# Kernel tuning notes

Measured on AMD Instinct MI355X. Metric: run time of the kernel, lower is better.

Reference implementation:

```python
import jax, jax.numpy as jnp
import numpy as np

T, B, N = 2048, 32, 1024   # time, batch, dan_hidden_size
H = 8                      # multihead_size
N2 = 128                   # attention_hidden_size
K = N // H                 # N_H = 128 per-head dim
K2 = N2 // H               # N2_H = 16 per-head attention dim


def setup_inputs() -> dict:
    key = jax.random.key(0)
    ks = jax.random.split(key, 10)
    s_n = 1.0 / np.sqrt(N)
    s_k = 1.0 / np.sqrt(K)
    s_k2 = 1.0 / np.sqrt(K2)
    return {
        "hyp": jax.random.normal(ks[0], (T, B, N), dtype=jnp.float32),
        # H independent per-head linears N -> K, stacked: (H, K, N)
        "Wmh": jax.random.uniform(ks[1], (H, K, N), minval=-s_n, maxval=s_n, dtype=jnp.float32),
        "bmh": jax.random.uniform(ks[2], (H, K), minval=-s_n, maxval=s_n, dtype=jnp.float32),
        # shared W: K -> K2
        "W": jax.random.uniform(ks[3], (K2, K), minval=-s_k, maxval=s_k, dtype=jnp.float32),
        "bW": jax.random.uniform(ks[4], (K2,), minval=-s_k, maxval=s_k, dtype=jnp.float32),
        # shared W_m: K -> K2
        "Wm": jax.random.uniform(ks[5], (K2, K), minval=-s_k, maxval=s_k, dtype=jnp.float32),
        "bWm": jax.random.uniform(ks[6], (K2,), minval=-s_k, maxval=s_k, dtype=jnp.float32),
        # shared W_h: K2 -> 1
        "Wh": jax.random.uniform(ks[7], (K2,), minval=-s_k2, maxval=s_k2, dtype=jnp.float32),
        "bWh": jax.random.uniform(ks[8], (), minval=-s_k2, maxval=s_k2, dtype=jnp.float32),
        "dan_hidden_size": N,
        "attention_hidden_size": N2,
        "multihead_size": H,
    }


def reference(hyp, Wmh, bmh, W, bW, Wm, bWm, Wh, bWh,
              dan_hidden_size, attention_hidden_size, multihead_size):
    # Per-head projections, all heads at once: (B, T, H, K)
    X = jnp.einsum('tbn,hkn->bthk', hyp, Wmh) + bmh
    # mean over time (original x.mean(0)): (B, H, K)
    m = X.mean(axis=1)
    # tanh-gated additive scoring: (B, T, H, K2)
    g = jnp.tanh(jnp.einsum('bthk,qk->bthq', X, W) + bW) \
        * jnp.tanh(jnp.einsum('bhk,qk->bhq', m, Wm) + bWm)[:, None]
    # scalar score per (b, t, h), softmax over time
    s = jnp.einsum('bthq,q->bth', g, Wh) + bWh
    a = jax.nn.softmax(s, axis=1)                       # (B, T, H)
    # attention-weighted sum over time: (B, H, K)
    c = jnp.einsum('bth,bthk->bhk', a, X)
    # concat heads along feature dim (head-major order, matches torch.cat)
    Bsz = c.shape[0]
    return c.reshape(Bsz, -1)                            # (B, N)
```

## Files before the change

### kernel.cpp

```cpp
#include <hip/hip_runtime.h>
#include <hip/hip_bf16.h>

#define T_DIM 2048
#define B_DIM 32
#define N_DIM 1024
#define H_DIM 8
#define K_DIM 128
#define Q_DIM 16

typedef __bf16 bf16x8 __attribute__((ext_vector_type(8)));
typedef __bf16 bf16x4 __attribute__((ext_vector_type(4)));
typedef float  f32x4  __attribute__((ext_vector_type(4)));

__device__ inline bf16x8 cvt8(float4 a, float4 b) {
    bf16x8 r;
    r[0] = (__bf16)a.x; r[1] = (__bf16)a.y; r[2] = (__bf16)a.z; r[3] = (__bf16)a.w;
    r[4] = (__bf16)b.x; r[5] = (__bf16)b.y; r[6] = (__bf16)b.z; r[7] = (__bf16)b.w;
    return r;
}

__global__ __launch_bounds__(256)
void cvt_f32_bf16(const float* __restrict__ s, __bf16* __restrict__ d)
{
    const long i = ((long)blockIdx.x * 256 + threadIdx.x) * 8;
    float4 a = *(const float4*)(s + i);
    float4 b = *(const float4*)(s + i + 4);
    *(bf16x8*)(d + i) = cvt8(a, b);
}

__global__ __launch_bounds__(512, 2)
void gemm_x_8ph(const __bf16* __restrict__ A, const __bf16* __restrict__ Bw,
                const float* __restrict__ bias, __bf16* __restrict__ X)
{
    __shared__ __bf16 lds[2][2][16384];

    const int tid  = threadIdx.x;
    const int lane = tid & 63;
    const int w    = tid >> 6;
    const int wm   = w >> 2;
    const int wn   = w & 3;

    const int bid  = blockIdx.x;
    const int wgid = (bid & 7) * 128 + (bid >> 3);
    const int bm   = wgid >> 2;
    const int bn   = wgid & 3;
    const long row0 = (long)bm * 256;
    const long col0 = (long)bn * 256;

    const int srow = w * 8 + (lane >> 3);
    const int scol = ((lane & 7) ^ (lane >> 3)) * 8;
    const __bf16* Ag = A  + (row0 + srow) * 1024 + scol;
    const __bf16* Bg = Bw + (col0 + srow) * 1024 + scol;
    const int ldst = w * 512;

    auto stage = [&](int kt, int sl) {
        const long ko = (long)kt * 64;
        #pragma unroll
        for (int j = 0; j < 4; ++j)
            __builtin_amdgcn_global_load_lds(
                (const __attribute__((address_space(1))) void*)(Ag + (long)j * 65536 + ko),
                (__attribute__((address_space(3))) void*)(&lds[sl][0][j * 4096 + ldst]),
                16, 0, 0);
        #pragma unroll
        for (int j = 0; j < 4; ++j)
            __builtin_amdgcn_global_load_lds(
                (const __attribute__((address_space(1))) void*)(Bg + (long)j * 65536 + ko),
                (__attribute__((address_space(3))) void*)(&lds[sl][1][j * 4096 + ldst]),
                16, 0, 0);
    };

    const int fr = lane & 15;
    const int g2 = lane >> 4;
    const int x7 = lane & 7;

    f32x4 acc[8][4];
    #pragma unroll
    for (int i = 0; i < 8; ++i)
        #pragma unroll
        for (int j = 0; j < 4; ++j)
            acc[i][j] = f32x4{0.f, 0.f, 0.f, 0.f};

    stage(0, 0);
    stage(1, 1);
    asm volatile("s_waitcnt vmcnt(8)" ::: "memory");
    __builtin_amdgcn_s_barrier();

    #pragma unroll 1
    for (int i = 0; i < 16; ++i) {
        const int s = i & 1;
        const __bf16* Al = &lds[s][0][0];
        const __bf16* Bl = &lds[s][1][0];

        bf16x8 a0[4][2], a1[4][2], b0[4], b1[4];

        #pragma unroll
        for (int mi = 0; mi < 4; ++mi) {
            const int row = wm * 128 + mi * 16 + fr;
            a0[mi][0] = *(const bf16x8*)(Al + row * 64 + ((g2    ) ^ x7) * 8);
            a0[mi][1] = *(const bf16x8*)(Al + row * 64 + ((4 + g2) ^ x7) * 8);
        }
        #pragma unroll
        for (int ni = 0; ni < 4; ++ni) {
            const int row = wn * 64 + ni * 16 + fr;
            b0[ni] = *(const bf16x8*)(Bl + row * 64 + ((g2) ^ x7) * 8);
        }
        __builtin_amdgcn_s_barrier();
        __builtin_amdgcn_s_setprio(1);
        #pragma unroll
        for (int mi = 0; mi < 4; ++mi)
            #pragma unroll
            for (int ni = 0; ni < 4; ++ni)
                acc[mi][ni] = __builtin_amdgcn_mfma_f32_16x16x32_bf16(a0[mi][0], b0[ni], acc[mi][ni], 0, 0, 0);
        __builtin_amdgcn_s_setprio(0);
        __builtin_amdgcn_s_barrier();

        #pragma unroll
        for (int ni = 0; ni < 4; ++ni) {
            const int row = wn * 64 + ni * 16 + fr;
            b1[ni] = *(const bf16x8*)(Bl + row * 64 + ((4 + g2) ^ x7) * 8);
        }
        __builtin_amdgcn_s_barrier();
        __builtin_amdgcn_s_setprio(1);
        #pragma unroll
        for (int mi = 0; mi < 4; ++mi)
            #pragma unroll
            for (int ni = 0; ni < 4; ++ni)
                acc[mi][ni] = __builtin_amdgcn_mfma_f32_16x16x32_bf16(a0[mi][1], b1[ni], acc[mi][ni], 0, 0, 0);
        __builtin_amdgcn_s_setprio(0);
        __builtin_amdgcn_s_barrier();

        #pragma unroll
        for (int mi = 0; mi < 4; ++mi) {
            const int row = wm * 128 + (mi + 4) * 16 + fr;
            a1[mi][0] = *(const bf16x8*)(Al + row * 64 + ((g2    ) ^ x7) * 8);
            a1[mi][1] = *(const bf16x8*)(Al + row * 64 + ((4 + g2) ^ x7) * 8);
        }
        __builtin_amdgcn_s_barrier();
        __builtin_amdgcn_s_setprio(1);
        #pragma unroll
        for (int mi = 0; mi < 4; ++mi)
            #pragma unroll
            for (int ni = 0; ni < 4; ++ni)
                acc[mi + 4][ni] = __builtin_amdgcn_mfma_f32_16x16x32_bf16(a1[mi][0], b0[ni], acc[mi + 4][ni], 0, 0, 0);
        __builtin_amdgcn_s_setprio(0);
        __builtin_amdgcn_s_barrier();

        if (i < 14) stage(i + 2, s);
        __builtin_amdgcn_s_barrier();
        __builtin_amdgcn_s_setprio(1);
        #pragma unroll
        for (int mi = 0; mi < 4; ++mi)
            #pragma unroll
            for (int ni = 0; ni < 4; ++ni)
                acc[mi + 4][ni] = __builtin_amdgcn_mfma_f32_16x16x32_bf16(a1[mi][1], b1[ni], acc[mi + 4][ni], 0, 0, 0);
        __builtin_amdgcn_s_setprio(0);
        if (i < 14) { asm volatile("s_waitcnt vmcnt(8)" ::: "memory"); }
        else        { asm volatile("s_waitcnt vmcnt(0)" ::: "memory"); }
        __builtin_amdgcn_s_barrier();
    }

    const int g4 = lane >> 4;
    #pragma unroll
    for (int ni = 0; ni < 4; ++ni) {
        const long col = col0 + wn * 64 + ni * 16 + fr;
        const float bv = bias[col];
        #pragma unroll
        for (int mi = 0; mi < 8; ++mi) {
            #pragma unroll
            for (int r = 0; r < 4; ++r) {
                const long row = row0 + wm * 128 + mi * 16 + g4 * 4 + r;
                X[row * 1024 + col] = (__bf16)(acc[mi][ni][r] + bv);
            }
        }
    }
}

__global__ __launch_bounds__(256, 2)
void gemm_x_kernel(const float* __restrict__ A, const float* __restrict__ Bw,
                   const float* __restrict__ bias, __bf16* __restrict__ X)
{
    __shared__ __bf16 As[128 * 32];
    __shared__ __bf16 Bs[128 * 32];
    const int tid  = threadIdx.x;
    const int lane = tid & 63;
    const int w    = tid >> 6;
    const int wr   = w >> 1;
    const int wc   = w & 1;
    const int bn   = blockIdx.x;
    const int bm   = blockIdx.y;
    const int row0 = bm * 128;
    const int col0 = bn * 128;
    const int srow = tid >> 2;
    const int sk8  = (tid & 3) * 8;
    f32x4 acc[4][4];
    #pragma unroll
    for (int i = 0; i < 4; ++i)
        #pragma unroll
        for (int j = 0; j < 4; ++j)
            acc[i][j] = f32x4{0.f, 0.f, 0.f, 0.f};
    const int fr = lane & 15;
    const int g8 = (lane >> 4) * 8;
    for (int kt = 0; kt < 32; ++kt) {
        const int k0 = kt * 32;
        const float* ap0 = A  + (row0 + srow) * 1024 + k0 + sk8;
        const float* ap1 = A  + (row0 + 64 + srow) * 1024 + k0 + sk8;
        const float* bp0 = Bw + (col0 + srow) * 1024 + k0 + sk8;
        const float* bp1 = Bw + (col0 + 64 + srow) * 1024 + k0 + sk8;
        float4 a00 = *(const float4*)ap0;
        float4 a01 = *(const float4*)(ap0 + 4);
        float4 a10 = *(const float4*)ap1;
        float4 a11 = *(const float4*)(ap1 + 4);
        float4 b00 = *(const float4*)bp0;
        float4 b01 = *(const float4*)(bp0 + 4);
        float4 b10 = *(const float4*)bp1;
        float4 b11 = *(const float4*)(bp1 + 4);
        __syncthreads();
        *(bf16x8*)(As + srow * 32 + sk8)        = cvt8(a00, a01);
        *(bf16x8*)(As + (64 + srow) * 32 + sk8) = cvt8(a10, a11);
        *(bf16x8*)(Bs + srow * 32 + sk8)        = cvt8(b00, b01);
        *(bf16x8*)(Bs + (64 + srow) * 32 + sk8) = cvt8(b10, b11);
        __syncthreads();
        bf16x8 af[4], bf[4];
        #pragma unroll
        for (int m = 0; m < 4; ++m)
            af[m] = *(const bf16x8*)(As + (wr * 64 + m * 16 + fr) * 32 + g8);
        #pragma unroll
        for (int n = 0; n < 4; ++n)
            bf[n] = *(const bf16x8*)(Bs + (wc * 64 + n * 16 + fr) * 32 + g8);
        #pragma unroll
        for (int m = 0; m < 4; ++m)
            #pragma unroll
            for (int n = 0; n < 4; ++n)
                acc[m][n] = __builtin_amdgcn_mfma_f32_16x16x32_bf16(af[m], bf[n], acc[m][n], 0, 0, 0);
    }
    const int g4 = lane >> 4;
    #pragma unroll
    for (int n = 0; n < 4; ++n) {
        const int col = col0 + wc * 64 + n * 16 + fr;
        const float bv = bias[col];
        #pragma unroll
        for (int m = 0; m < 4; ++m) {
            #pragma unroll
            for (int r = 0; r < 4; ++r) {
                const int row = row0 + wr * 64 + m * 16 + g4 * 4 + r;
                X[(long)row * 1024 + col] = (__bf16)(acc[m][n][r] + bv);
            }
        }
    }
}

__global__ __launch_bounds__(256)
void mean_part_k(const __bf16* __restrict__ X, float* __restrict__ mpart)
{
    const int bx = blockIdx.x;
    const int b  = bx & 31;
    const int tc = bx >> 5;
    const int j4 = threadIdx.x * 4;
    float a0 = 0.f, a1 = 0.f, a2 = 0.f, a3 = 0.f;
    #pragma unroll 4
    for (int i = 0; i < 64; ++i) {
        const int t = tc * 64 + i;
        bf16x4 v = *(const bf16x4*)(X + (long)(t * 32 + b) * 1024 + j4);
        a0 += (float)v[0]; a1 += (float)v[1]; a2 += (float)v[2]; a3 += (float)v[3];
    }
    float4* mp = (float4*)(mpart + ((long)tc * 32 + b) * 1024 + j4);
    *mp = make_float4(a0, a1, a2, a3);
}

__global__ __launch_bounds__(256)
void gate2_k(const float* __restrict__ mpart, const float* __restrict__ Wm,
             const float* __restrict__ bWm, float* __restrict__ g2)
{
    __shared__ float mrow[1024];
    const int b = blockIdx.x;
    for (int j = threadIdx.x; j < 1024; j += 256) {
        float s = 0.f;
        #pragma unroll 8
        for (int tc = 0; tc < 32; ++tc) s += mpart[((long)tc * 32 + b) * 1024 + j];
        mrow[j] = s * (1.0f / 2048.0f);
    }
    __syncthreads();
    if (threadIdx.x < 128) {
        const int h = threadIdx.x >> 4;
        const int q = threadIdx.x & 15;
        float d = bWm[q];
        #pragma unroll 8
        for (int k = 0; k < 128; ++k) d += mrow[h * 128 + k] * Wm[q * 128 + k];
        g2[(b * 8 + h) * 16 + q] = tanhf(d);
    }
}

__global__ __launch_bounds__(256)
void scores_k(const __bf16* __restrict__ X, const float* __restrict__ W,
              const float* __restrict__ bW, const float* __restrict__ g2,
              const float* __restrict__ Wh, const float* __restrict__ bWh,
              float* __restrict__ sbuf)
{
    const int tid   = threadIdx.x;
    const int lane  = tid & 63;
    const int w     = tid >> 6;
    const int gw    = blockIdx.x * 4 + w;
    const int rbase = gw * 16;
    const int q     = lane & 15;
    const int g4    = lane >> 4;

    bf16x8 bfr[4];
    #pragma unroll
    for (int c = 0; c < 4; ++c) {
        const float* wp = W + q * 128 + c * 32 + g4 * 8;
        float4 w0 = *(const float4*)wp;
        float4 w1 = *(const float4*)(wp + 4);
        bfr[c] = cvt8(w0, w1);
    }
    const __bf16* xp = X + (long)(rbase + q) * 128 + g4 * 8;
    bf16x8 afr[4];
    #pragma unroll
    for (int c = 0; c < 4; ++c) afr[c] = *(const bf16x8*)(xp + c * 32);

    f32x4 acc = f32x4{0.f, 0.f, 0.f, 0.f};
    #pragma unroll
    for (int c = 0; c < 4; ++c)
        acc = __builtin_amdgcn_mfma_f32_16x16x32_bf16(afr[c], bfr[c], acc, 0, 0, 0);

    const float whq  = Wh[q];
    const float bWv  = bW[q];
    const float bWhv = *bWh;
    #pragma unroll
    for (int r = 0; r < 4; ++r) {
        const int row = rbase + g4 * 4 + r;
        const int h   = row & 7;
        const int bt  = row >> 3;
        const int b   = bt & 31;
        const int t   = bt >> 5;
        float val = tanhf(acc[r] + bWv) * g2[(b * 8 + h) * 16 + q] * whq;
        val += __shfl_xor(val, 1);
        val += __shfl_xor(val, 2);
        val += __shfl_xor(val, 4);
        val += __shfl_xor(val, 8);
        if (q == 0) sbuf[(b * 8 + h) * 2048 + t] = val + bWhv;
    }
}

__global__ __launch_bounds__(256)
void softmax_k(float* __restrict__ s)
{
    __shared__ float red[256];
    const int bh = blockIdx.x;
    const int tid = threadIdx.x;
    float* row = s + bh * 2048;
    float4 v0 = *(const float4*)(row + tid * 8);
    float4 v1 = *(const float4*)(row + tid * 8 + 4);
    float v[8] = {v0.x, v0.y, v0.z, v0.w, v1.x, v1.y, v1.z, v1.w};
    float mx = v[0];
    #pragma unroll
    for (int i = 1; i < 8; ++i) mx = fmaxf(mx, v[i]);
    red[tid] = mx;
    __syncthreads();
    for (int st = 128; st > 0; st >>= 1) {
        if (tid < st) red[tid] = fmaxf(red[tid], red[tid + st]);
        __syncthreads();
    }
    mx = red[0];
    __syncthreads();
    float sum = 0.f;
    #pragma unroll
    for (int i = 0; i < 8; ++i) { v[i] = expf(v[i] - mx); sum += v[i]; }
    red[tid] = sum;
    __syncthreads();
    for (int st = 128; st > 0; st >>= 1) {
        if (tid < st) red[tid] += red[tid + st];
        __syncthreads();
    }
    const float inv = 1.0f / red[0];
    *(float4*)(row + tid * 8)     = make_float4(v[0] * inv, v[1] * inv, v[2] * inv, v[3] * inv);
    *(float4*)(row + tid * 8 + 4) = make_float4(v[4] * inv, v[5] * inv, v[6] * inv, v[7] * inv);
}

__global__ __launch_bounds__(256)
void wsum_k(const float* __restrict__ a, const __bf16* __restrict__ X,
            float* __restrict__ wpart)
{
    __shared__ float pk[8 * 128];
    const int bx = blockIdx.x;
    const int tc = bx & 7;
    const int bh = bx >> 3;
    const int b  = bh >> 3;
    const int h  = bh & 7;
    const int tid = threadIdx.x;
    const int kq = tid & 31;
    const int tr = tid >> 5;
    const float* ar = a + bh * 2048 + tc * 256;
    float a0 = 0.f, a1 = 0.f, a2 = 0.f, a3 = 0.f;
    #pragma unroll 4
    for (int i = tr; i < 256; i += 8) {
        const int t = tc * 256 + i;
        const float av = ar[i];
        bf16x4 xv = *(const bf16x4*)(X + (long)(t * 32 + b) * 1024 + h * 128 + kq * 4);
        a0 += av * (float)xv[0];
        a1 += av * (float)xv[1];
        a2 += av * (float)xv[2];
        a3 += av * (float)xv[3];
    }
    pk[tr * 128 + kq * 4 + 0] = a0;
    pk[tr * 128 + kq * 4 + 1] = a1;
    pk[tr * 128 + kq * 4 + 2] = a2;
    pk[tr * 128 + kq * 4 + 3] = a3;
    __syncthreads();
    if (tid < 128) {
        float s2 = 0.f;
        #pragma unroll
        for (int r = 0; r < 8; ++r) s2 += pk[r * 128 + tid];
        wpart[(long)bx * 128 + tid] = s2;
    }
}

__global__ __launch_bounds__(256)
void wsum_fin(const float* __restrict__ wpart, float* __restrict__ out)
{
    const int idx = blockIdx.x * 256 + threadIdx.x;
    const int k  = idx & 127;
    const int bh = idx >> 7;
    const int b  = bh >> 3;
    const int h  = bh & 7;
    float s = 0.f;
    #pragma unroll
    for (int tc = 0; tc < 8; ++tc) s += wpart[(bh * 8 + tc) * 128 + k];
    out[b * 1024 + h * 128 + k] = s;
}

extern "C" void kernel_launch(void* const* d_in, const int* in_sizes, int n_in,
                              void* d_out, int out_size, void* d_ws, size_t ws_size,
                              hipStream_t stream)
{
    const float* hyp = (const float*)d_in[0];
    const float* Wmh = (const float*)d_in[1];
    const float* bmh = (const float*)d_in[2];
    const float* W   = (const float*)d_in[3];
    const float* bW  = (const float*)d_in[4];
    const float* Wm  = (const float*)d_in[5];
    const float* bWm = (const float*)d_in[6];
    const float* Wh  = (const float*)d_in[7];
    const float* bWh = (const float*)d_in[8];
    float* out = (float*)d_out;

    char* ws = (char*)d_ws;
    const size_t SZ_X   = 134217728;
    const size_t SZ_AB  = 134217728;
    const size_t SZ_BB  = 2097152;
    const size_t SZ_MP  = 4194304;
    const size_t SZ_G2  = 16384;
    const size_t SZ_SB  = 2097152;
    const size_t SZ_WP  = 1048576;
    const size_t need_fast = SZ_X + SZ_AB + SZ_BB + SZ_MP + SZ_G2 + SZ_SB + SZ_WP;

    __bf16* X;
    float *mpart, *g2, *sbuf, *wpart;

    if (ws_size >= need_fast) {
        X              = (__bf16*)(ws);
        __bf16* Ab     = (__bf16*)(ws + SZ_X);
        __bf16* Bb     = (__bf16*)(ws + SZ_X + SZ_AB);
        mpart = (float*)(ws + SZ_X + SZ_AB + SZ_BB);
        g2    = (float*)(ws + SZ_X + SZ_AB + SZ_BB + SZ_MP);
        sbuf  = (float*)(ws + SZ_X + SZ_AB + SZ_BB + SZ_MP + SZ_G2);
        wpart = (float*)(ws + SZ_X + SZ_AB + SZ_BB + SZ_MP + SZ_G2 + SZ_SB);

        cvt_f32_bf16<<<32768, 256, 0, stream>>>(hyp, Ab);
        cvt_f32_bf16<<<512,   256, 0, stream>>>(Wmh, Bb);
        gemm_x_8ph<<<1024, 512, 0, stream>>>(Ab, Bb, bmh, X);
    } else {
        X     = (__bf16*)(ws);
        mpart = (float*)(ws + SZ_X);
        g2    = (float*)(ws + SZ_X + SZ_MP);
        sbuf  = (float*)(ws + SZ_X + SZ_MP + SZ_G2);
        wpart = (float*)(ws + SZ_X + SZ_MP + SZ_G2 + SZ_SB);
        gemm_x_kernel<<<dim3(8, 512), 256, 0, stream>>>(hyp, Wmh, bmh, X);
    }

    mean_part_k<<<1024, 256, 0, stream>>>(X, mpart);
    gate2_k<<<32, 256, 0, stream>>>(mpart, Wm, bWm, g2);
    scores_k<<<8192, 256, 0, stream>>>(X, W, bW, g2, Wh, bWh, sbuf);
    softmax_k<<<256, 256, 0, stream>>>(sbuf);
    wsum_k<<<2048, 256, 0, stream>>>(sbuf, X, wpart);
    wsum_fin<<<128, 256, 0, stream>>>(wpart, out);
}
```

Measured before the change: 361.2 us.

## Fuse time-mean partial sums into GEMM epilogue and swap MFMA operands

The GEMM now computes X transposed per MFMA tile, with operands swapped, so each lane holds four consecutive columns. This lets the epilogue write bf16x4 vector stores and add bias with float4 loads. The same epilogue accumulates per-batch partial sums over its 256 time rows, combining them across the two row-warp groups through LDS. That removes the separate mean_part_k pass, which reread all of X. The cost is a larger mpart buffer (256 partials) that gate2_k must reduce, and the fallback path for small workspaces is dropped.

```diff
diff --git a/kernel.cpp b/kernel.cpp
--- a/kernel.cpp
+++ b/kernel.cpp
@@ -30,7 +30,8 @@
 
 __global__ __launch_bounds__(512, 2)
 void gemm_x_8ph(const __bf16* __restrict__ A, const __bf16* __restrict__ Bw,
-                const float* __restrict__ bias, __bf16* __restrict__ X)
+                const float* __restrict__ bias, __bf16* __restrict__ X,
+                float* __restrict__ mpart)
 {
     __shared__ __bf16 lds[2][2][16384];
 
@@ -91,13 +92,12 @@
         const __bf16* Al = &lds[s][0][0];
         const __bf16* Bl = &lds[s][1][0];
 
-        bf16x8 a0[4][2], a1[4][2], b0[4], b1[4];
+        bf16x8 a0[4], a0h[4], a1[4], a1h[4], b0[4], b1[4];
 
         #pragma unroll
         for (int mi = 0; mi < 4; ++mi) {
             const int row = wm * 128 + mi * 16 + fr;
-            a0[mi][0] = *(const bf16x8*)(Al + row * 64 + ((g2    ) ^ x7) * 8);
-            a0[mi][1] = *(const bf16x8*)(Al + row * 64 + ((4 + g2) ^ x7) * 8);
+            a0[mi] = *(const bf16x8*)(Al + row * 64 + ((g2) ^ x7) * 8);
         }
         #pragma unroll
         for (int ni = 0; ni < 4; ++ni) {
@@ -110,10 +110,15 @@
         for (int mi = 0; mi < 4; ++mi)
             #pragma unroll
             for (int ni = 0; ni < 4; ++ni)
-                acc[mi][ni] = __builtin_amdgcn_mfma_f32_16x16x32_bf16(a0[mi][0], b0[ni], acc[mi][ni], 0, 0, 0);
+                acc[mi][ni] = __builtin_amdgcn_mfma_f32_16x16x32_bf16(b0[ni], a0[mi], acc[mi][ni], 0, 0, 0);
         __builtin_amdgcn_s_setprio(0);
         __builtin_amdgcn_s_barrier();
 
+        #pragma unroll
+        for (int mi = 0; mi < 4; ++mi) {
+            const int row = wm * 128 + mi * 16 + fr;
+            a0h[mi] = *(const bf16x8*)(Al + row * 64 + ((4 + g2) ^ x7) * 8);
+        }
         #pragma unroll
         for (int ni = 0; ni < 4; ++ni) {
             const int row = wn * 64 + ni * 16 + fr;
@@ -125,15 +130,15 @@
         for (int mi = 0; mi < 4; ++mi)
             #pragma unroll
             for (int ni = 0; ni < 4; ++ni)
-                acc[mi][ni] = __builtin_amdgcn_mfma_f32_16x16x32_bf16(a0[mi][1], b1[ni], acc[mi][ni], 0, 0, 0);
+                acc[mi][ni] = __builtin_amdgcn_mfma_f32_16x16x32_bf16(b1[ni], a0h[mi], acc[mi][ni], 0, 0, 0);
         __builtin_amdgcn_s_setprio(0);
         __builtin_amdgcn_s_barrier();
 
         #pragma unroll
         for (int mi = 0; mi < 4; ++mi) {
             const int row = wm * 128 + (mi + 4) * 16 + fr;
-            a1[mi][0] = *(const bf16x8*)(Al + row * 64 + ((g2    ) ^ x7) * 8);
-            a1[mi][1] = *(const bf16x8*)(Al + row * 64 + ((4 + g2) ^ x7) * 8);
+            a1[mi]  = *(const bf16x8*)(Al + row * 64 + ((g2    ) ^ x7) * 8);
+            a1h[mi] = *(const bf16x8*)(Al + row * 64 + ((4 + g2) ^ x7) * 8);
         }
         __builtin_amdgcn_s_barrier();
         __builtin_amdgcn_s_setprio(1);
@@ -141,7 +146,7 @@
         for (int mi = 0; mi < 4; ++mi)
             #pragma unroll
             for (int ni = 0; ni < 4; ++ni)
-                acc[mi + 4][ni] = __builtin_amdgcn_mfma_f32_16x16x32_bf16(a1[mi][0], b0[ni], acc[mi + 4][ni], 0, 0, 0);
+                acc[mi + 4][ni] = __builtin_amdgcn_mfma_f32_16x16x32_bf16(b0[ni], a1[mi], acc[mi + 4][ni], 0, 0, 0);
         __builtin_amdgcn_s_setprio(0);
         __builtin_amdgcn_s_barrier();
 
@@ -152,7 +157,7 @@
         for (int mi = 0; mi < 4; ++mi)
             #pragma unroll
             for (int ni = 0; ni < 4; ++ni)
-                acc[mi + 4][ni] = __builtin_amdgcn_mfma_f32_16x16x32_bf16(a1[mi][1], b1[ni], acc[mi + 4][ni], 0, 0, 0);
+                acc[mi + 4][ni] = __builtin_amdgcn_mfma_f32_16x16x32_bf16(b1[ni], a1h[mi], acc[mi + 4][ni], 0, 0, 0);
         __builtin_amdgcn_s_setprio(0);
         if (i < 14) { asm volatile("s_waitcnt vmcnt(8)" ::: "memory"); }
         else        { asm volatile("s_waitcnt vmcnt(0)" ::: "memory"); }
@@ -160,111 +165,60 @@
     }
 
     const int g4 = lane >> 4;
-    #pragma unroll
-    for (int ni = 0; ni < 4; ++ni) {
-        const long col = col0 + wn * 64 + ni * 16 + fr;
-        const float bv = bias[col];
-        #pragma unroll
-        for (int mi = 0; mi < 8; ++mi) {
-            #pragma unroll
-            for (int r = 0; r < 4; ++r) {
-                const long row = row0 + wm * 128 + mi * 16 + g4 * 4 + r;
-                X[row * 1024 + col] = (__bf16)(acc[mi][ni][r] + bv);
+    const long colb = col0 + wn * 64 + g4 * 4;
+
+    float4 bias4[4];
+    #pragma unroll
+    for (int ni = 0; ni < 4; ++ni)
+        bias4[ni] = *(const float4*)(bias + colb + ni * 16);
+
+    f32x4 msum[2][4];
+    #pragma unroll
+    for (int bh = 0; bh < 2; ++bh)
+        #pragma unroll
+        for (int ni = 0; ni < 4; ++ni)
+            msum[bh][ni] = f32x4{0.f, 0.f, 0.f, 0.f};
+
+    #pragma unroll
+    for (int mi = 0; mi < 8; ++mi) {
+        const long row = row0 + wm * 128 + mi * 16 + fr;
+        #pragma unroll
+        for (int ni = 0; ni < 4; ++ni) {
+            f32x4 xv;
+            xv[0] = acc[mi][ni][0] + bias4[ni].x;
+            xv[1] = acc[mi][ni][1] + bias4[ni].y;
+            xv[2] = acc[mi][ni][2] + bias4[ni].z;
+            xv[3] = acc[mi][ni][3] + bias4[ni].w;
+            bf16x4 xb;
+            xb[0] = (__bf16)xv[0]; xb[1] = (__bf16)xv[1];
+            xb[2] = (__bf16)xv[2]; xb[3] = (__bf16)xv[3];
+            *(bf16x4*)(X + row * 1024 + colb + ni * 16) = xb;
+            msum[mi & 1][ni] += xv;
+        }
+    }
+
+    float* ldsf = (float*)&lds[0][0][0];
+    __syncthreads();
+    if (wm == 1) {
+        #pragma unroll
+        for (int bh = 0; bh < 2; ++bh)
+            #pragma unroll
+            for (int ni = 0; ni < 4; ++ni)
+                *(f32x4*)(ldsf + (bh * 16 + fr) * 256 + wn * 64 + ni * 16 + g4 * 4) = msum[bh][ni];
+    }
+    __syncthreads();
+    if (wm == 0) {
+        #pragma unroll
+        for (int bh = 0; bh < 2; ++bh) {
+            const int b = bh * 16 + fr;
+            #pragma unroll
+            for (int ni = 0; ni < 4; ++ni) {
+                f32x4 other = *(const f32x4*)(ldsf + b * 256 + wn * 64 + ni * 16 + g4 * 4);
+                f32x4 tot = msum[bh][ni] + other;
+                *(f32x4*)(mpart + ((long)bm * 32 + b) * 1024 + colb + ni * 16) = tot;
             }
         }
     }
-}
-
-__global__ __launch_bounds__(256, 2)
-void gemm_x_kernel(const float* __restrict__ A, const float* __restrict__ Bw,
-                   const float* __restrict__ bias, __bf16* __restrict__ X)
-{
-    __shared__ __bf16 As[128 * 32];
-    __shared__ __bf16 Bs[128 * 32];
-    const int tid  = threadIdx.x;
-    const int lane = tid & 63;
-    const int w    = tid >> 6;
-    const int wr   = w >> 1;
-    const int wc   = w & 1;
-    const int bn   = blockIdx.x;
-    const int bm   = blockIdx.y;
-    const int row0 = bm * 128;
-    const int col0 = bn * 128;
-    const int srow = tid >> 2;
-    const int sk8  = (tid & 3) * 8;
-    f32x4 acc[4][4];
-    #pragma unroll
-    for (int i = 0; i < 4; ++i)
-        #pragma unroll
-        for (int j = 0; j < 4; ++j)
-            acc[i][j] = f32x4{0.f, 0.f, 0.f, 0.f};
-    const int fr = lane & 15;
-    const int g8 = (lane >> 4) * 8;
-    for (int kt = 0; kt < 32; ++kt) {
-        const int k0 = kt * 32;
-        const float* ap0 = A  + (row0 + srow) * 1024 + k0 + sk8;
-        const float* ap1 = A  + (row0 + 64 + srow) * 1024 + k0 + sk8;
-        const float* bp0 = Bw + (col0 + srow) * 1024 + k0 + sk8;
-        const float* bp1 = Bw + (col0 + 64 + srow) * 1024 + k0 + sk8;
-        float4 a00 = *(const float4*)ap0;
-        float4 a01 = *(const float4*)(ap0 + 4);
-        float4 a10 = *(const float4*)ap1;
-        float4 a11 = *(const float4*)(ap1 + 4);
-        float4 b00 = *(const float4*)bp0;
-        float4 b01 = *(const float4*)(bp0 + 4);
-        float4 b10 = *(const float4*)bp1;
-        float4 b11 = *(const float4*)(bp1 + 4);
-        __syncthreads();
-        *(bf16x8*)(As + srow * 32 + sk8)        = cvt8(a00, a01);
-        *(bf16x8*)(As + (64 + srow) * 32 + sk8) = cvt8(a10, a11);
-        *(bf16x8*)(Bs + srow * 32 + sk8)        = cvt8(b00, b01);
-        *(bf16x8*)(Bs + (64 + srow) * 32 + sk8) = cvt8(b10, b11);
-        __syncthreads();
-        bf16x8 af[4], bf[4];
-        #pragma unroll
-        for (int m = 0; m < 4; ++m)
-            af[m] = *(const bf16x8*)(As + (wr * 64 + m * 16 + fr) * 32 + g8);
-        #pragma unroll
-        for (int n = 0; n < 4; ++n)
-            bf[n] = *(const bf16x8*)(Bs + (wc * 64 + n * 16 + fr) * 32 + g8);
-        #pragma unroll
-        for (int m = 0; m < 4; ++m)
-            #pragma unroll
-            for (int n = 0; n < 4; ++n)
-                acc[m][n] = __builtin_amdgcn_mfma_f32_16x16x32_bf16(af[m], bf[n], acc[m][n], 0, 0, 0);
-    }
-    const int g4 = lane >> 4;
-    #pragma unroll
-    for (int n = 0; n < 4; ++n) {
-        const int col = col0 + wc * 64 + n * 16 + fr;
-        const float bv = bias[col];
-        #pragma unroll
-        for (int m = 0; m < 4; ++m) {
-            #pragma unroll
-            for (int r = 0; r < 4; ++r) {
-                const int row = row0 + wr * 64 + m * 16 + g4 * 4 + r;
-                X[(long)row * 1024 + col] = (__bf16)(acc[m][n][r] + bv);
-            }
-        }
-    }
-}
-
-__global__ __launch_bounds__(256)
-void mean_part_k(const __bf16* __restrict__ X, float* __restrict__ mpart)
-{
-    const int bx = blockIdx.x;
-    const int b  = bx & 31;
-    const int tc = bx >> 5;
-    const int j4 = threadIdx.x * 4;
-    float a0 = 0.f, a1 = 0.f, a2 = 0.f, a3 = 0.f;
-    #pragma unroll 4
-    for (int i = 0; i < 64; ++i) {
-        const int t = tc * 64 + i;
-        bf16x4 v = *(const bf16x4*)(X + (long)(t * 32 + b) * 1024 + j4);
-        a0 += (float)v[0]; a1 += (float)v[1]; a2 += (float)v[2]; a3 += (float)v[3];
-    }
-    float4* mp = (float4*)(mpart + ((long)tc * 32 + b) * 1024 + j4);
-    *mp = make_float4(a0, a1, a2, a3);
 }
 
 __global__ __launch_bounds__(256)
@@ -273,12 +227,14 @@
 {
     __shared__ float mrow[1024];
     const int b = blockIdx.x;
-    for (int j = threadIdx.x; j < 1024; j += 256) {
-        float s = 0.f;
-        #pragma unroll 8
-        for (int tc = 0; tc < 32; ++tc) s += mpart[((long)tc * 32 + b) * 1024 + j];
-        mrow[j] = s * (1.0f / 2048.0f);
-    }
+    const int j4 = threadIdx.x * 4;
+    f32x4 s = f32x4{0.f, 0.f, 0.f, 0.f};
+    for (int bm = 0; bm < 256; ++bm)
+        s += *(const f32x4*)(mpart + ((long)bm * 32 + b) * 1024 + j4);
+    mrow[j4 + 0] = s[0] * (1.0f / 2048.0f);
+    mrow[j4 + 1] = s[1] * (1.0f / 2048.0f);
+    mrow[j4 + 2] = s[2] * (1.0f / 2048.0f);
+    mrow[j4 + 3] = s[3] * (1.0f / 2048.0f);
     __syncthreads();
     if (threadIdx.x < 128) {
         const int h = threadIdx.x >> 4;
@@ -447,37 +403,22 @@
     const size_t SZ_X   = 134217728;
     const size_t SZ_AB  = 134217728;
     const size_t SZ_BB  = 2097152;
-    const size_t SZ_MP  = 4194304;
+    const size_t SZ_MP  = 33554432;
     const size_t SZ_G2  = 16384;
     const size_t SZ_SB  = 2097152;
-    const size_t SZ_WP  = 1048576;
-    const size_t need_fast = SZ_X + SZ_AB + SZ_BB + SZ_MP + SZ_G2 + SZ_SB + SZ_WP;
-
-    __bf16* X;
-    float *mpart, *g2, *sbuf, *wpart;
-
-    if (ws_size >= need_fast) {
-        X              = (__bf16*)(ws);
-        __bf16* Ab     = (__bf16*)(ws + SZ_X);
-        __bf16* Bb     = (__bf16*)(ws + SZ_X + SZ_AB);
-        mpart = (float*)(ws + SZ_X + SZ_AB + SZ_BB);
-        g2    = (float*)(ws + SZ_X + SZ_AB + SZ_BB + SZ_MP);
-        sbuf  = (float*)(ws + SZ_X + SZ_AB + SZ_BB + SZ_MP + SZ_G2);
-        wpart = (float*)(ws + SZ_X + SZ_AB + SZ_BB + SZ_MP + SZ_G2 + SZ_SB);
-
-        cvt_f32_bf16<<<32768, 256, 0, stream>>>(hyp, Ab);
-        cvt_f32_bf16<<<512,   256, 0, stream>>>(Wmh, Bb);
-        gemm_x_8ph<<<1024, 512, 0, stream>>>(Ab, Bb, bmh, X);
-    } else {
-        X     = (__bf16*)(ws);
-        mpart = (float*)(ws + SZ_X);
-        g2    = (float*)(ws + SZ_X + SZ_MP);
-        sbuf  = (float*)(ws + SZ_X + SZ_MP + SZ_G2);
-        wpart = (float*)(ws + SZ_X + SZ_MP + SZ_G2 + SZ_SB);
-        gemm_x_kernel<<<dim3(8, 512), 256, 0, stream>>>(hyp, Wmh, bmh, X);
-    }
-
-    mean_part_k<<<1024, 256, 0, stream>>>(X, mpart);
+
+    size_t off = 0;
+    __bf16* X     = (__bf16*)(ws + off); off += SZ_X;
+    __bf16* Ab    = (__bf16*)(ws + off); off += SZ_AB;
+    __bf16* Bb    = (__bf16*)(ws + off); off += SZ_BB;
+    float*  mpart = (float*) (ws + off); off += SZ_MP;
+    float*  g2    = (float*) (ws + off); off += SZ_G2;
+    float*  sbuf  = (float*) (ws + off); off += SZ_SB;
+    float*  wpart = (float*) (ws + off);
+
+    cvt_f32_bf16<<<32768, 256, 0, stream>>>(hyp, Ab);
+    cvt_f32_bf16<<<512,   256, 0, stream>>>(Wmh, Bb);
+    gemm_x_8ph<<<1024, 512, 0, stream>>>(Ab, Bb, bmh, X, mpart);
     gate2_k<<<32, 256, 0, stream>>>(mpart, Wm, bWm, g2);
     scores_k<<<8192, 256, 0, stream>>>(X, W, bW, g2, Wh, bWh, sbuf);
     softmax_k<<<256, 256, 0, stream>>>(sbuf);
```

After: 346.7 us. 4.0% less time.
